# Kernel optimization log

Hardware: AMD Instinct MI355X
Metric: run time of the kernel (lower is better)

The kernel has to match this reference:

```python
import jax, jax.numpy as jnp
import numpy as np
from jax import lax

ITER_ = 3
SMOOTH = 1e-05

B, C, D, H, W = 2, 3, 128, 160, 160


def _maxpool_axis(x, axis):
    # 3-wide max pool along one axis, stride 1, pad 1 (torch pads with -inf for max pool)
    win = [1] * x.ndim
    win[axis] = 3
    pad = [(0, 0)] * x.ndim
    pad[axis] = (1, 1)
    return lax.reduce_window(x, -jnp.inf, lax.max, tuple(win), (1,) * x.ndim, tuple(pad))


def _soft_erode(x):
    # min over axis-aligned erosions (erode = -maxpool(-x))
    nx = -x
    p1 = -_maxpool_axis(nx, 2)
    p2 = -_maxpool_axis(nx, 3)
    p3 = -_maxpool_axis(nx, 4)
    return jnp.minimum(jnp.minimum(p1, p2), p3)


def _soft_dilate(x):
    pad = ((0, 0), (0, 0), (1, 1), (1, 1), (1, 1))
    return lax.reduce_window(x, -jnp.inf, lax.max, (1, 1, 3, 3, 3), (1,) * 5, pad)


def _soft_open(x):
    return _soft_dilate(_soft_erode(x))


def _soft_skel(x):
    skel = jax.nn.relu(x - _soft_open(x))
    x_work = x
    for _ in range(ITER_):
        x_work = _soft_erode(x_work)
        delta = jax.nn.relu(x_work - _soft_open(x_work))
        skel = skel + jax.nn.relu(delta - skel * delta)
    return skel


def setup_inputs() -> dict:
    key = jax.random.key(0)
    k1, k2 = jax.random.split(key)
    net_output = jax.random.uniform(k1, (B, C, D, H, W), dtype=jnp.float32)
    target = jax.random.randint(k2, (B, 1, D, H, W), 0, C, dtype=jnp.int64)
    return {"net_output": net_output, "target": target}


def reference(net_output, target):
    num_classes = net_output.shape[1]
    labels = jnp.clip(target[:, 0], 0, num_classes - 1)
    target_1h = jax.nn.one_hot(labels, num_classes, dtype=net_output.dtype)  # [B,D,H,W,C]
    target_1h = jnp.moveaxis(target_1h, -1, 1)  # [B,C,D,H,W]

    # include_background=False, num_classes > 1 -> drop background channel
    pred = net_output[:, 1:]
    gt = target_1h[:, 1:]

    skel_pred = _soft_skel(pred)
    skel_gt = _soft_skel(gt)

    dims = (2, 3, 4)
    tprec = (jnp.sum(skel_pred * gt, dims) + SMOOTH) / (jnp.sum(skel_pred, dims) + SMOOTH)
    tsens = (jnp.sum(skel_gt * pred, dims) + SMOOTH) / (jnp.sum(skel_gt, dims) + SMOOTH)
    cl_dice = (2.0 * tprec * tsens + SMOOTH) / (tprec + tsens + SMOOTH)
    return 1.0 - jnp.mean(cl_dice)
```

## Files before the change

### kernel.cpp

```cpp
#include <hip/hip_runtime.h>
#include <math.h>

#define D_ 128
#define H_ 160
#define W_ 160
#define HW_ (H_ * W_)
#define V_ (D_ * H_ * W_)
#define SMOOTHF 1e-5

#define R_ 16
#define TY 10
#define ZC 16
#define COLS 40
#define NT 640
#define LROW 41
#define NYT 16
#define NZC 8
#define NTB (NYT * NZC)

__device__ __forceinline__ float max3f(float a, float b, float c) { return fmaxf(fmaxf(a, b), c); }
__device__ __forceinline__ float min3f(float a, float b, float c) { return fminf(fminf(a, b), c); }
__device__ __forceinline__ float4 f4min(float4 a, float4 b) {
    return make_float4(fminf(a.x,b.x), fminf(a.y,b.y), fminf(a.z,b.z), fminf(a.w,b.w));
}
__device__ __forceinline__ float4 f4max(float4 a, float4 b) {
    return make_float4(fmaxf(a.x,b.x), fmaxf(a.y,b.y), fmaxf(a.z,b.z), fmaxf(a.w,b.w));
}
__device__ __forceinline__ float4 min3x(float l, float4 c, float r) {
    return make_float4(min3f(l,c.x,c.y), min3f(c.x,c.y,c.z), min3f(c.y,c.z,c.w), min3f(c.z,c.w,r));
}
__device__ __forceinline__ float4 max3x(float l, float4 c, float r) {
    return make_float4(max3f(l,c.x,c.y), max3f(c.x,c.y,c.z), max3f(c.y,c.z,c.w), max3f(c.z,c.w,r));
}
__device__ __forceinline__ float4 relu4sub(float4 a, float4 b) {
    return make_float4(fmaxf(a.x-b.x,0.f), fmaxf(a.y-b.y,0.f), fmaxf(a.z-b.z,0.f), fmaxf(a.w-b.w,0.f));
}
__device__ __forceinline__ float4 skel_upd(float4 s, float4 d) {
    return make_float4(s.x + fmaxf(d.x - s.x*d.x, 0.f), s.y + fmaxf(d.y - s.y*d.y, 0.f),
                       s.z + fmaxf(d.z - s.z*d.z, 0.f), s.w + fmaxf(d.w - s.w*d.w, 0.f));
}

__device__ __forceinline__ float4 load_src4(const float* __restrict__ net,
                                            const int* __restrict__ tgt,
                                            int i, long p) {
    if (i < 4) {
        int b = i >> 1, c = (i & 1) + 1;
        return *(const float4*)(net + (long)(b * 3 + c) * V_ + p);
    } else {
        int j = i - 4;
        int b = j >> 1, c = (j & 1) + 1;
        int4 t = *(const int4*)(tgt + (long)b * V_ + p);
        float4 o;
        int tx = t.x < 0 ? 0 : (t.x > 2 ? 2 : t.x);
        int ty = t.y < 0 ? 0 : (t.y > 2 ? 2 : t.y);
        int tz = t.z < 0 ? 0 : (t.z > 2 ? 2 : t.z);
        int tw = t.w < 0 ? 0 : (t.w > 2 ? 2 : t.w);
        o.x = (tx == c) ? 1.0f : 0.0f;
        o.y = (ty == c) ? 1.0f : 0.0f;
        o.z = (tz == c) ? 1.0f : 0.0f;
        o.w = (tw == c) ? 1.0f : 0.0f;
        return o;
    }
}

template <int VAR>
__global__ __launch_bounds__(NT, 4) void fused_pair(
    const float* __restrict__ net, const int* __restrict__ tgt, int i0,
    const float* __restrict__ e_in, float* __restrict__ e_out,
    float* __restrict__ skel, float* __restrict__ partials) {

    __shared__ float4 Pb[2][R_ * LROW];
    __shared__ float4 E1b[2][R_ * LROW];
    __shared__ float4 E2b[2][R_ * LROW];
    __shared__ float smr[NT / 64][2];

    const int j = blockIdx.y, i = i0 + j;
    const int bx = blockIdx.x;
    const int y0 = (bx % NYT) * TY;
    const int z0 = (bx / NYT) * ZC;
    const int tid = threadIdx.x;
    const int r  = tid / COLS;
    const int x4 = tid - r * COLS;
    const int y  = y0 - 3 + r;
    const bool yok  = (y >= 0 && y < H_);
    const bool ymok = (y - 1 >= 0 && y - 1 < H_);
    const bool ypok = (y + 1 >= 0 && y + 1 < H_);
    const int rm = (r > 0) ? r - 1 : 0;
    const int rp = (r < R_ - 1) ? r + 1 : R_ - 1;
    const int xm = (x4 > 0) ? x4 - 1 : 0;
    const int xp = (x4 < COLS - 1) ? x4 + 1 : COLS - 1;
    const bool fxm = (x4 > 0), fxp = (x4 < COLS - 1);
    const bool rout = (r >= 3 && r < 3 + TY);
    const long colbase = (long)(yok ? y : 0) * W_ + x4 * 4;

    const float* ein_v = (VAR == 1) ? e_in + (long)j * V_ : nullptr;
    float* eout_v = (VAR == 0) ? e_out + (long)j * V_ : nullptr;
    float* skel_v = skel + (long)j * V_;
    const int ipart = (i < 4) ? (i + 4) : (i - 4);

    const float4 INF4  = make_float4( INFINITY,  INFINITY,  INFINITY,  INFINITY);
    const float4 NINF4 = make_float4(-INFINITY, -INFINITY, -INFINITY, -INFINITY);

    float4 p1 = INF4, p2 = INF4;
    float4 b1 = NINF4, b2 = NINF4, b3 = NINF4;
    float4 c1 = NINF4;
    float4 x1a = NINF4, x1b = NINF4, x1c = NINF4;
    float4 x2a = NINF4, x2b = NINF4;
    float acc0 = 0.f, acc1 = 0.f;

    for (int s = z0 - 3; s <= z0 + ZC + 3; ++s) {
        float4 anew = INF4;
        if (s <= z0 + ZC + 2) {
            const bool zok = (s >= 0 && s < D_);
            if (zok && yok) {
                long p = (long)s * HW_ + colbase;
                anew = (VAR == 0) ? load_src4(net, tgt, i, p)
                                  : *(const float4*)(ein_v + p);
            }
            Pb[s & 1][r * LROW + x4] = anew;
        }

        float4 fe1 = NINF4;
        if (s >= z0 - 1 && s <= z0 + ZC + 2) {
            const int z1 = s - 1;
            const bool z1ok = (z1 >= 0 && z1 < D_);
            const float4* Pp = Pb[z1 & 1];
            float4 up = Pp[rm * LROW + x4];
            float4 dn = Pp[rp * LROW + x4];
            float lf = Pp[r * LROW + xm].w;
            float rt = Pp[r * LROW + xp].x;
            if (!ymok) up = INF4;
            if (!ypok) dn = INF4;
            if (!fxm) lf = INFINITY;
            if (!fxp) rt = INFINITY;
            float4 e = f4min(f4min(min3x(lf, p1, rt), f4min(up, dn)), f4min(p2, anew));
            if (!z1ok || !yok) e = NINF4;
            fe1 = e;
            E1b[z1 & 1][r * LROW + x4] = e;
        }

        float4 fe2 = NINF4, f1 = NINF4;
        if (s >= z0 + 1 && s <= z0 + ZC + 2) {
            const int z2 = s - 2;
            const bool z2ok = (z2 >= 0 && z2 < D_);
            const float4* Ep = E1b[z2 & 1];
            float4 n01 = Ep[rm * LROW + x4];
            float4 n21 = Ep[rp * LROW + x4];
            float4 c = b1;
            float l0 = fxm ? Ep[rm * LROW + xm].w : -INFINITY;
            float r0 = fxp ? Ep[rm * LROW + xp].x : -INFINITY;
            float l1 = fxm ? Ep[r  * LROW + xm].w : -INFINITY;
            float r1 = fxp ? Ep[r  * LROW + xp].x : -INFINITY;
            float l2 = fxm ? Ep[rp * LROW + xm].w : -INFINITY;
            float r2 = fxp ? Ep[rp * LROW + xp].x : -INFINITY;
            {
                float4 up = ymok ? n01 : INF4;
                float4 dn = ypok ? n21 : INF4;
                float lf = fxm ? l1 : INFINITY;
                float rt = fxp ? r1 : INFINITY;
                float4 zu = (z2 >= 1)     ? b2  : INF4;
                float4 zd = (z2 + 1 < D_) ? fe1 : INF4;
                float4 e = f4min(f4min(min3x(lf, c, rt), f4min(up, dn)), f4min(zu, zd));
                if (!z2ok || !yok) e = NINF4;
                fe2 = e;
            }
            {
                float4 m = f4max(f4max(max3x(l0, n01, r0), max3x(l1, c, r1)), max3x(l2, n21, r2));
                if (!z2ok) m = NINF4;
                f1 = m;
            }
            E2b[z2 & 1][r * LROW + x4] = fe2;
            if (VAR == 0 && z2 >= z0 && z2 < z0 + ZC && rout) {
                *(float4*)(eout_v + (long)z2 * HW_ + colbase) = fe2;
            }
        }

        float4 f2 = NINF4;
        if (s >= z0 + 2) {
            const int z3 = s - 3;
            const float4* Eq = E2b[z3 & 1];
            float4 m01 = Eq[rm * LROW + x4];
            float4 m21 = Eq[rp * LROW + x4];
            float l0 = fxm ? Eq[rm * LROW + xm].w : -INFINITY;
            float r0 = fxp ? Eq[rm * LROW + xp].x : -INFINITY;
            float l1 = fxm ? Eq[r  * LROW + xm].w : -INFINITY;
            float r1 = fxp ? Eq[r  * LROW + xp].x : -INFINITY;
            float l2 = fxm ? Eq[rp * LROW + xm].w : -INFINITY;
            float r2 = fxp ? Eq[rp * LROW + xp].x : -INFINITY;
            f2 = f4max(f4max(max3x(l0, m01, r0), max3x(l1, c1, r1)), max3x(l2, m21, r2));
        }

        {
            const int z = s - 4;
            if (z >= z0 && z < z0 + ZC && rout) {
                float4 dil1 = f4max(f4max(x1a, x1b), x1c);
                float4 dil2 = f4max(f4max(x2a, x2b), f2);
                float4 ce1 = b3;
                long p = (long)z * HW_ + colbase;
                if (VAR == 0) {
                    float4 cin = load_src4(net, tgt, i, p);
                    float4 s0 = relu4sub(cin, dil1);
                    float4 d1 = relu4sub(ce1, dil2);
                    *(float4*)(skel_v + p) = skel_upd(s0, d1);
                } else {
                    float4 cin = *(const float4*)(ein_v + p);
                    float4 psk = *(const float4*)(skel_v + p);
                    float4 ppr = load_src4(net, tgt, ipart, p);
                    float4 d2 = relu4sub(cin, dil1);
                    float4 sp = skel_upd(psk, d2);
                    float4 d3 = relu4sub(ce1, dil2);
                    float4 fin = skel_upd(sp, d3);
                    acc0 += fin.x * ppr.x + fin.y * ppr.y + fin.z * ppr.z + fin.w * ppr.w;
                    acc1 += fin.x + fin.y + fin.z + fin.w;
                }
            }
        }

        p2 = p1; p1 = anew;
        b3 = b2; b2 = b1; b1 = fe1;
        c1 = fe2;
        x1a = x1b; x1b = x1c; x1c = f1;
        x2a = x2b; x2b = f2;

        __syncthreads();
    }

    if (VAR == 1) {
        #pragma unroll
        for (int off = 32; off > 0; off >>= 1) {
            acc0 += __shfl_down(acc0, off);
            acc1 += __shfl_down(acc1, off);
        }
        int wid = tid >> 6, lane = tid & 63;
        __syncthreads();
        if (lane == 0) { smr[wid][0] = acc0; smr[wid][1] = acc1; }
        __syncthreads();
        if (tid == 0) {
            float t0 = 0.f, t1 = 0.f;
            #pragma unroll
            for (int w = 0; w < NT / 64; ++w) { t0 += smr[w][0]; t1 += smr[w][1]; }
            long base = ((long)i * NTB + bx) * 2;
            partials[base + 0] = t0;
            partials[base + 1] = t1;
        }
    }
}

__global__ void reduce_partials_kernel(const float* __restrict__ partials,
                                       int i0,
                                       double* __restrict__ sums) {
    int i = i0 + blockIdx.x;
    int t = threadIdx.x;
    long base = ((long)i * NTB + t) * 2;
    double v0 = (double)partials[base + 0];
    double v1 = (double)partials[base + 1];
    #pragma unroll
    for (int off = 32; off > 0; off >>= 1) {
        v0 += __shfl_down(v0, off);
        v1 += __shfl_down(v1, off);
    }
    __shared__ double sm[2][2];
    int wid = t >> 6, lane = t & 63;
    if (lane == 0) { sm[wid][0] = v0; sm[wid][1] = v1; }
    __syncthreads();
    if (t == 0) {
        sums[2 * i + 0] = sm[0][0] + sm[1][0];
        sums[2 * i + 1] = sm[0][1] + sm[1][1];
    }
}

__global__ void finalize_kernel(const double* __restrict__ sums,
                                float* __restrict__ out) {
    if (threadIdx.x == 0 && blockIdx.x == 0) {
        double acc = 0.0;
        #pragma unroll
        for (int i = 0; i < 4; ++i) {
            double tprec = (sums[2 * i + 0] + SMOOTHF) / (sums[2 * i + 1] + SMOOTHF);
            double tsens = (sums[2 * (i + 4) + 0] + SMOOTHF) / (sums[2 * (i + 4) + 1] + SMOOTHF);
            double cl = (2.0 * tprec * tsens + SMOOTHF) / (tprec + tsens + SMOOTHF);
            acc += cl;
        }
        out[0] = (float)(1.0 - acc * 0.25);
    }
}

extern "C" void kernel_launch(void* const* d_in, const int* in_sizes, int n_in,
                              void* d_out, int out_size, void* d_ws, size_t ws_size,
                              hipStream_t stream) {
    const float* net = (const float*)d_in[0];
    const int* tgt = (const int*)d_in[1];
    float* out = (float*)d_out;

    char* ws = (char*)d_ws;
    double* sums = (double*)ws;
    float* partials = (float*)(ws + 256);
    size_t head = 256 + (size_t)8 * NTB * 2 * sizeof(float);
    head = (head + 255) & ~(size_t)255;
    float* base = (float*)(ws + head);

    size_t perVol = (size_t)2 * V_ * sizeof(float);
    int G = 1;
    if (ws_size >= head + perVol * 8) G = 8;
    else if (ws_size >= head + perVol * 4) G = 4;
    else if (ws_size >= head + perVol * 2) G = 2;

    dim3 blk(NT);
    dim3 grd(NTB, G);

    for (int i0 = 0; i0 < 8; i0 += G) {
        float* SKEL = base;
        float* E2buf = base + (size_t)G * V_;

        fused_pair<0><<<grd, blk, 0, stream>>>(net, tgt, i0, nullptr, E2buf, SKEL, nullptr);
        fused_pair<1><<<grd, blk, 0, stream>>>(net, tgt, i0, E2buf, nullptr, SKEL, partials);

        reduce_partials_kernel<<<G, 128, 0, stream>>>(partials, i0, sums);
    }

    finalize_kernel<<<1, 64, 0, stream>>>(sums, out);
}
```

Baseline: 345.7 us.

## Double z-chunk depth and prefetch next slice load one step ahead

Doubles the z-chunk size per block (ZC 16→32, NZC 8→4), which halves the grid and cuts the fraction of halo slices recomputed per chunk. Adds a software prefetch so the global load for slice s+1 is issued before the current slice's shared-memory stencil work, hiding memory latency. The partial-reduction kernel shrinks to a single wavefront because NTB is now 64, which removes its shared-memory step and barrier. The trade-offs are fewer blocks for occupancy and an extra live float4 register per thread.

```diff
diff --git a/kernel.cpp b/kernel.cpp
--- a/kernel.cpp
+++ b/kernel.cpp
@@ -10,12 +10,12 @@
 
 #define R_ 16
 #define TY 10
-#define ZC 16
+#define ZC 32
 #define COLS 40
 #define NT 640
 #define LROW 41
 #define NYT 16
-#define NZC 8
+#define NZC 4
 #define NTB (NYT * NZC)
 
 __device__ __forceinline__ float max3f(float a, float b, float c) { return fmaxf(fmaxf(a, b), c); }
@@ -108,16 +108,30 @@
     float4 x2a = NINF4, x2b = NINF4;
     float acc0 = 0.f, acc1 = 0.f;
 
+    float4 a_inflight = INF4;
+    {
+        const int sf = z0 - 3;
+        if (sf >= 0 && sf < D_ && yok) {
+            long p = (long)sf * HW_ + colbase;
+            a_inflight = (VAR == 0) ? load_src4(net, tgt, i, p)
+                                    : *(const float4*)(ein_v + p);
+        }
+    }
+
     for (int s = z0 - 3; s <= z0 + ZC + 3; ++s) {
-        float4 anew = INF4;
+        float4 anew = a_inflight;
         if (s <= z0 + ZC + 2) {
-            const bool zok = (s >= 0 && s < D_);
-            if (zok && yok) {
-                long p = (long)s * HW_ + colbase;
-                anew = (VAR == 0) ? load_src4(net, tgt, i, p)
-                                  : *(const float4*)(ein_v + p);
-            }
             Pb[s & 1][r * LROW + x4] = anew;
+        }
+        {
+            const int sn = s + 1;
+            float4 v = INF4;
+            if (sn <= z0 + ZC + 2 && sn >= 0 && sn < D_ && yok) {
+                long p = (long)sn * HW_ + colbase;
+                v = (VAR == 0) ? load_src4(net, tgt, i, p)
+                               : *(const float4*)(ein_v + p);
+            }
+            a_inflight = v;
         }
 
         float4 fe1 = NINF4;
@@ -259,13 +273,9 @@
         v0 += __shfl_down(v0, off);
         v1 += __shfl_down(v1, off);
     }
-    __shared__ double sm[2][2];
-    int wid = t >> 6, lane = t & 63;
-    if (lane == 0) { sm[wid][0] = v0; sm[wid][1] = v1; }
-    __syncthreads();
     if (t == 0) {
-        sums[2 * i + 0] = sm[0][0] + sm[1][0];
-        sums[2 * i + 1] = sm[0][1] + sm[1][1];
+        sums[2 * i + 0] = v0;
+        sums[2 * i + 1] = v1;
     }
 }
 
@@ -314,7 +324,7 @@
         fused_pair<0><<<grd, blk, 0, stream>>>(net, tgt, i0, nullptr, E2buf, SKEL, nullptr);
         fused_pair<1><<<grd, blk, 0, stream>>>(net, tgt, i0, E2buf, nullptr, SKEL, partials);
 
-        reduce_partials_kernel<<<G, 128, 0, stream>>>(partials, i0, sums);
+        reduce_partials_kernel<<<G, 64, 0, stream>>>(partials, i0, sums);
     }
 
     finalize_kernel<<<1, 64, 0, stream>>>(sums, out);
```

Result: faster. 318.9 us (-7.8%).
